# Kernel tuning notes

Measured on AMD Instinct MI355X. Metric: run time of the kernel, lower is better.

## Reference

```python
import jax, jax.numpy as jnp
import numpy as np

BLK = 64          # BLOCK_M == BLOCK_N == 64
TOPK_RATIO = 0.25


def _block_map(q, k, topk):
    # mean_pool of q blocks and mean-centered k blocks, then top-k key blocks per query block
    B, H, L, D = q.shape
    nb = L // BLK
    k_cent = k - jnp.mean(k, axis=-2, keepdims=True)
    pq = q.reshape(B, H, nb, BLK, D).mean(axis=3)          # [B,H,Mb,D]
    pk = k_cent.reshape(B, H, nb, BLK, D).mean(axis=3)     # [B,H,Nb,D]
    score = jnp.einsum('bhmd,bhnd->bhmn', pq, pk)
    _, lut = jax.lax.top_k(score, topk)                    # [B,H,Mb,topk] int32
    return lut


def reference(q, k, v):
    B, H, L, D = q.shape
    nb = L // BLK                       # M_BLOCKS == N_BLOCKS (L divisible by 64)
    topk = min(nb, int(TOPK_RATIO * nb))
    qk_scale = D ** (-0.5)

    lut = jax.lax.stop_gradient(_block_map(q, k, topk))    # routing is non-differentiable

    qb = q.reshape(B, H, nb, BLK, D)
    kb = k.reshape(B, H, nb, BLK, D)
    vb = v.reshape(B, H, nb, BLK, D)

    # gather selected key/value blocks per query block: [B,H,Mb,topk,BLK,D]
    idx = lut[:, :, :, :, None, None]
    k_sel = jnp.take_along_axis(kb[:, :, None], idx, axis=3)
    v_sel = jnp.take_along_axis(vb[:, :, None], idx, axis=3)

    # block-sparse attention restricted to the selected blocks
    s = jnp.einsum('bhmqd,bhmtkd->bhmqtk', qb, k_sel) * qk_scale
    s = s.reshape(B, H, nb, BLK, topk * BLK)
    p = jax.nn.softmax(s, axis=-1)                         # online-softmax equivalent
    v_flat = v_sel.reshape(B, H, nb, topk * BLK, D)
    o = jnp.einsum('bhmqn,bhmnd->bhmqd', p, v_flat)
    return o.reshape(B, H, L, D)


def setup_inputs() -> dict:
    key = jax.random.key(0)
    k1, k2, k3 = jax.random.split(key, 3)
    shape = (2, 8, 4096, 64)
    return {
        'q': jax.random.normal(k1, shape, dtype=jnp.float32),
        'k': jax.random.normal(k2, shape, dtype=jnp.float32),
        'v': jax.random.normal(k3, shape, dtype=jnp.float32),
    }
```

## Files before the change

### kernel.cpp

```cpp
#include <hip/hip_runtime.h>
#include <hip/hip_bf16.h>

#define B_ 2
#define H_ 8
#define L_ 4096
#define D_ 64
#define NB_ 64
#define TOPK_ 16
#define BH_ 16

typedef __bf16 bf16x8 __attribute__((ext_vector_type(8)));
typedef float f32x4 __attribute__((ext_vector_type(4)));

#if __has_builtin(__builtin_amdgcn_exp2f)
#define EXP2(x) __builtin_amdgcn_exp2f(x)
#else
#define EXP2(x) exp2f(x)
#endif

__device__ __forceinline__ void async_copy16(void* lds, const void* g) {
  __builtin_amdgcn_global_load_lds(
      (const __attribute__((address_space(1))) void*)g,
      (__attribute__((address_space(3))) void*)lds, 16, 0, 0);
}

__global__ __launch_bounds__(256) void prep_all_kernel(
    const float* __restrict__ q, const float* __restrict__ k,
    const float* __restrict__ v,
    float* __restrict__ pq, float* __restrict__ pk,
    __bf16* __restrict__ kswz, __bf16* __restrict__ vimg) {
  const int tid = threadIdx.x;
  if (blockIdx.x < BH_ * NB_) {
    const int blk = blockIdx.x;
    const int bh = blk >> 6, m = blk & 63;
    const int d = tid & 63, g = tid >> 6;
    const float* qb = q + ((size_t)bh * L_ + m * 64 + g * 16) * D_ + d;
    float sq = 0.f;
#pragma unroll
    for (int i = 0; i < 16; i++) sq += qb[(size_t)i * D_];
    __shared__ float bufq[4][64];
    bufq[g][d] = sq;
    __syncthreads();
    if (g == 0) {
      float tq = bufq[0][d] + bufq[1][d] + bufq[2][d] + bufq[3][d];
      pq[(size_t)blk * 64 + d] = tq * (1.f / 64.f);
    }
  } else if (blockIdx.x < 2 * BH_ * NB_) {
    const int blk = blockIdx.x - BH_ * NB_;
    const int srow = tid >> 2;
    const int sc16 = (tid & 3) * 16;
    __shared__ __align__(16) float s_kf[64][64];

    const float* ks = k + (size_t)blk * 4096 + srow * 64 + sc16;
    float kf[16];
#pragma unroll
    for (int h = 0; h < 4; h++) {
      float4 t4 = *(const float4*)(ks + h * 4);
      kf[h * 4 + 0] = t4.x; kf[h * 4 + 1] = t4.y; kf[h * 4 + 2] = t4.z; kf[h * 4 + 3] = t4.w;
      *(float4*)&s_kf[srow][sc16 + h * 4] = t4;
    }

    __bf16* gk = kswz + (size_t)blk * 4096;
#pragma unroll
    for (int h = 0; h < 2; h++) {
      int c8 = (sc16 >> 3) + h;
      bf16x8 kw;
#pragma unroll
      for (int j = 0; j < 8; j++) kw[j] = (__bf16)kf[h * 8 + j];
      *(bf16x8*)(gk + srow * 64 + ((c8 ^ (srow & 7)) << 3)) = kw;
    }
    __syncthreads();

    const int d = tid & 63, g = tid >> 6;
    float sk = 0.f;
#pragma unroll
    for (int i = 0; i < 16; i++) sk += s_kf[g * 16 + i][d];
    __shared__ float bufk[4][64];
    bufk[g][d] = sk;
    __syncthreads();
    if (g == 0) {
      float tk = bufk[0][d] + bufk[1][d] + bufk[2][d] + bufk[3][d];
      pk[(size_t)blk * 64 + d] = tk * (1.f / 64.f);
    }
  } else {
    const int blk = blockIdx.x - 2 * BH_ * NB_;
    const int srow = tid >> 2;
    const int sc16 = (tid & 3) * 16;

    const float* vs = v + (size_t)blk * 4096 + srow * 64 + sc16;
    float vf[16];
#pragma unroll
    for (int h = 0; h < 4; h++) {
      float4 u4 = *(const float4*)(vs + h * 4);
      vf[h * 4 + 0] = u4.x; vf[h * 4 + 1] = u4.y; vf[h * 4 + 2] = u4.z; vf[h * 4 + 3] = u4.w;
    }

    const int kpos = (srow & 32) + ((srow >> 2) & 3) * 8 + ((srow >> 4) & 1) * 4 + (srow & 3);
    __shared__ __align__(16) __bf16 s_vt[4096];
#pragma unroll
    for (int i = 0; i < 16; i++) {
      int d = sc16 + i;
      s_vt[d * 64 + kpos] = (__bf16)vf[i];
    }
    __syncthreads();
    __bf16* gv = vimg + (size_t)blk * 4096;
#pragma unroll
    for (int h = 0; h < 2; h++) {
      int c = tid + h * 256;
      int i = c >> 6, ln = c & 63;
      int ct2 = i & 3, s2 = i >> 2;
      int d = ct2 * 16 + (ln & 15), c8 = s2 * 4 + (ln >> 4);
      *(bf16x8*)(gv + c * 8) = *(const bf16x8*)(s_vt + d * 64 + c8 * 8);
    }
  }
}

__global__ __launch_bounds__(256) void blockmap_kernel(
    const float* __restrict__ pq, const float* __restrict__ pk,
    int* __restrict__ lut) {
  const int g = blockIdx.x;
  const int bh = g >> 2, q4 = g & 3;
  const int t = threadIdx.x;
  const int lane = t & 63, w = t >> 6;

  __shared__ float s_pk[64][65];
  __shared__ float s_km[64];
  __shared__ float s_pq[16][64];
  __shared__ float s_sc[4][64];

#pragma unroll
  for (int i = 0; i < 16; i++) {
    int idx = i * 256 + t;
    s_pk[idx >> 6][idx & 63] = pk[(size_t)bh * 4096 + idx];
  }
#pragma unroll
  for (int i = 0; i < 4; i++) {
    int idx = i * 256 + t;
    s_pq[idx >> 6][idx & 63] = pq[(size_t)bh * 4096 + q4 * 1024 + idx];
  }
  __syncthreads();
  if (t < 64) {
    float s = 0.f;
#pragma unroll 8
    for (int r = 0; r < 64; r++) s += s_pk[r][t];
    s_km[t] = s * (1.f / 64.f);
  }
  __syncthreads();

#pragma unroll
  for (int rr = 0; rr < 4; rr++) {
    const int row = w * 4 + rr;
    float sc = 0.f;
#pragma unroll 8
    for (int d2 = 0; d2 < 64; ++d2)
      sc += s_pq[row][d2] * (s_pk[lane][d2] - s_km[d2]);
    s_sc[w][lane] = sc;
    __syncthreads();
    int rank = 0;
#pragma unroll 8
    for (int j = 0; j < 64; j++) {
      float o = s_sc[w][j];
      rank += (o > sc) || (o == sc && j < lane);
    }
    if (rank < TOPK_)
      lut[((size_t)bh * 64 + q4 * 16 + row) * TOPK_ + rank] = lane;
    __syncthreads();
  }
}

__global__ __launch_bounds__(256) void sparse_attn_fast(
    const float* __restrict__ q, const __bf16* __restrict__ kswz,
    const __bf16* __restrict__ vimg, const float* __restrict__ pq,
    const float* __restrict__ pk, float* __restrict__ out) {
  const int bid = blockIdx.x;
  const int blk = (bid & 7) * 128 + (bid >> 3);
  const int bh = blk >> 6, m = blk & 63;
  const int tid = threadIdx.x;
  const int lane = tid & 63;
  const int w = tid >> 6;
  const int l16 = lane & 15, lhi = lane >> 4;

  __shared__ __align__(16) __bf16 Kb[2][2][4096];
  __shared__ float s_km[64];
  __shared__ float s_pqr[64];
  __shared__ float s_sc[64];
  __shared__ int s_lut[TOPK_];

  {
    float (*s_pk)[65] = (float(*)[65]) & Kb[0][0][0];
    const float* pkb = pk + (size_t)bh * 4096;
#pragma unroll
    for (int i = 0; i < 16; i++) {
      int idx = i * 256 + tid;
      s_pk[idx >> 6][idx & 63] = pkb[idx];
    }
    if (tid < 64) s_pqr[tid] = pq[((size_t)bh * 64 + m) * 64 + tid];
    __syncthreads();
    if (tid < 64) {
      float s = 0.f;
#pragma unroll 8
      for (int r = 0; r < 64; r++) s += s_pk[r][tid];
      s_km[tid] = s * (1.f / 64.f);
    }
    __syncthreads();
    float sc = 0.f;
#pragma unroll 8
    for (int d2 = 0; d2 < 64; ++d2)
      sc += s_pqr[d2] * (s_pk[lane][d2] - s_km[d2]);
    s_sc[lane] = sc;
    __syncthreads();
    int rank = 0;
#pragma unroll 8
    for (int j = 0; j < 64; j++) {
      float o = s_sc[j];
      rank += (o > sc) || (o == sc && j < lane);
    }
    if (rank < TOPK_) s_lut[rank] = lane;
    __syncthreads();
  }

  const size_t base = (size_t)bh * L_ * D_;
  const __bf16* kimg = kswz + (size_t)bh * 64 * 4096;
  const __bf16* vbase = vimg + (size_t)bh * 64 * 4096;

  const float QSC = 0.125f * 1.44269504088896340736f;
  bf16x8 qf[2];
  {
    const float* qrow = q + base + (size_t)(m * 64 + w * 16 + l16) * D_;
#pragma unroll
    for (int s = 0; s < 2; s++) {
      const float* p0 = qrow + s * 32 + lhi * 8;
      float4 a = *(const float4*)p0;
      float4 b = *(const float4*)(p0 + 4);
      bf16x8 f;
      f[0] = (__bf16)(a.x * QSC); f[1] = (__bf16)(a.y * QSC);
      f[2] = (__bf16)(a.z * QSC); f[3] = (__bf16)(a.w * QSC);
      f[4] = (__bf16)(b.x * QSC); f[5] = (__bf16)(b.y * QSC);
      f[6] = (__bf16)(b.z * QSC); f[7] = (__bf16)(b.w * QSC);
      qf[s] = f;
    }
  }

  f32x4 acc_o[4];
#pragma unroll
  for (int i = 0; i < 4; i++) acc_o[i] = (f32x4){0.f, 0.f, 0.f, 0.f};
  float l_run = 0.f;

  auto stagePair = [&](int b, int ka, int kb2) {
    const __bf16* g0 = kimg + (size_t)ka * 4096;
    const __bf16* g1 = kimg + (size_t)kb2 * 4096;
    async_copy16(&Kb[b][0][0 * 2048 + w * 512], g0 + 0 * 2048 + tid * 8);
    async_copy16(&Kb[b][0][1 * 2048 + w * 512], g0 + 1 * 2048 + tid * 8);
    async_copy16(&Kb[b][1][0 * 2048 + w * 512], g1 + 0 * 2048 + tid * 8);
    async_copy16(&Kb[b][1][1 * 2048 + w * 512], g1 + 1 * 2048 + tid * 8);
  };

  stagePair(0, s_lut[0], s_lut[1]);
  __syncthreads();

  for (int i = 0; i < 8; ++i) {
    const int cur = i & 1;
    if (i) __builtin_amdgcn_s_barrier();

    const int ka = s_lut[2 * i], kb2 = s_lut[2 * i + 1];

    const __bf16* gv0 = vbase + (size_t)ka * 4096 + lane * 8;
    bf16x8 vf0[8];
#pragma unroll
    for (int j = 0; j < 8; j++) vf0[j] = *(const bf16x8*)(gv0 + j * 512);

    asm volatile("s_waitcnt vmcnt(8)" ::: "memory");

    {
      const __bf16* Kl = &Kb[cur][0][0];
      f32x4 accs[4];
#pragma unroll
      for (int x = 0; x < 4; x++) accs[x] = (f32x4){0.f, 0.f, 0.f, 0.f};
      __builtin_amdgcn_s_setprio(1);
#pragma unroll
      for (int ct = 0; ct < 4; ct++) {
        const int key = ct * 16 + l16;
#pragma unroll
        for (int s = 0; s < 2; s++) {
          const int c8 = s * 4 + lhi;
          bf16x8 bk = *(const bf16x8*)&Kl[key * 64 + ((c8 ^ (key & 7)) << 3)];
          accs[ct] = __builtin_amdgcn_mfma_f32_16x16x32_bf16(bk, qf[s], accs[ct], 0, 0, 0);
        }
      }
      __builtin_amdgcn_s_setprio(0);
      bf16x8 pa0, pa1;
      float ls0 = 0.f, ls1 = 0.f;
#pragma unroll
      for (int j = 0; j < 8; j++) {
        float e0 = EXP2(accs[(j >> 2)][j & 3]);
        float e1 = EXP2(accs[2 + (j >> 2)][j & 3]);
        pa0[j] = (__bf16)e0; pa1[j] = (__bf16)e1;
        ls0 += e0; ls1 += e1;
      }
      l_run += ls0 + ls1;
      __builtin_amdgcn_s_setprio(1);
#pragma unroll
      for (int ct2 = 0; ct2 < 4; ct2++) {
        acc_o[ct2] = __builtin_amdgcn_mfma_f32_16x16x32_bf16(pa0, vf0[ct2], acc_o[ct2], 0, 0, 0);
        acc_o[ct2] = __builtin_amdgcn_mfma_f32_16x16x32_bf16(pa1, vf0[4 + ct2], acc_o[ct2], 0, 0, 0);
      }
      __builtin_amdgcn_s_setprio(0);
    }

    const __bf16* gv1 = vbase + (size_t)kb2 * 4096 + lane * 8;
    bf16x8 vf1[8];
#pragma unroll
    for (int j = 0; j < 8; j++) vf1[j] = *(const bf16x8*)(gv1 + j * 512);

    if (i + 1 < 8) stagePair(cur ^ 1, s_lut[2 * i + 2], s_lut[2 * i + 3]);

    {
      const __bf16* Kl = &Kb[cur][1][0];
      f32x4 accs[4];
#pragma unroll
      for (int x = 0; x < 4; x++) accs[x] = (f32x4){0.f, 0.f, 0.f, 0.f};
      __builtin_amdgcn_s_setprio(1);
#pragma unroll
      for (int ct = 0; ct < 4; ct++) {
        const int key = ct * 16 + l16;
#pragma unroll
        for (int s = 0; s < 2; s++) {
          const int c8 = s * 4 + lhi;
          bf16x8 bk = *(const bf16x8*)&Kl[key * 64 + ((c8 ^ (key & 7)) << 3)];
          accs[ct] = __builtin_amdgcn_mfma_f32_16x16x32_bf16(bk, qf[s], accs[ct], 0, 0, 0);
        }
      }
      __builtin_amdgcn_s_setprio(0);
      bf16x8 pa0, pa1;
      float ls0 = 0.f, ls1 = 0.f;
#pragma unroll
      for (int j = 0; j < 8; j++) {
        float e0 = EXP2(accs[(j >> 2)][j & 3]);
        float e1 = EXP2(accs[2 + (j >> 2)][j & 3]);
        pa0[j] = (__bf16)e0; pa1[j] = (__bf16)e1;
        ls0 += e0; ls1 += e1;
      }
      l_run += ls0 + ls1;
      __builtin_amdgcn_s_setprio(1);
#pragma unroll
      for (int ct2 = 0; ct2 < 4; ct2++) {
        acc_o[ct2] = __builtin_amdgcn_mfma_f32_16x16x32_bf16(pa0, vf1[ct2], acc_o[ct2], 0, 0, 0);
        acc_o[ct2] = __builtin_amdgcn_mfma_f32_16x16x32_bf16(pa1, vf1[4 + ct2], acc_o[ct2], 0, 0, 0);
      }
      __builtin_amdgcn_s_setprio(0);
    }
  }

  l_run += __shfl_xor(l_run, 16, 64);
  l_run += __shfl_xor(l_run, 32, 64);
  float rq[4];
#pragma unroll
  for (int r = 0; r < 4; r++)
    rq[r] = 1.f / __shfl(l_run, (lane & 48) | (lhi * 4 + r), 64);

  float* ob = out + base + (size_t)(m * 64 + w * 16) * D_;
#pragma unroll
  for (int ct2 = 0; ct2 < 4; ct2++) {
#pragma unroll
    for (int r = 0; r < 4; r++) {
      const int row = lhi * 4 + r, col = ct2 * 16 + l16;
      ob[(size_t)row * D_ + col] = acc_o[ct2][r] * rq[r];
    }
  }
}

__global__ __launch_bounds__(256) void block_means_kernel(
    const float* __restrict__ q, const float* __restrict__ k,
    float* __restrict__ pq, float* __restrict__ pk) {
  const int blk = blockIdx.x;
  const int bh = blk >> 6, m = blk & 63;
  const int d = threadIdx.x & 63, g = threadIdx.x >> 6;
  const float* qb = q + ((size_t)bh * L_ + m * 64 + g * 16) * D_ + d;
  const float* kb = k + ((size_t)bh * L_ + m * 64 + g * 16) * D_ + d;
  float sq = 0.f, sk = 0.f;
#pragma unroll
  for (int i = 0; i < 16; i++) { sq += qb[(size_t)i * D_]; sk += kb[(size_t)i * D_]; }
  __shared__ float bufq[4][64];
  __shared__ float bufk[4][64];
  bufq[g][d] = sq; bufk[g][d] = sk;
  __syncthreads();
  if (g == 0) {
    float tq = bufq[0][d] + bufq[1][d] + bufq[2][d] + bufq[3][d];
    float tk = bufk[0][d] + bufk[1][d] + bufk[2][d] + bufk[3][d];
    pq[(size_t)blk * 64 + d] = tq * (1.f / 64.f);
    pk[(size_t)blk * 64 + d] = tk * (1.f / 64.f);
  }
}

__global__ __launch_bounds__(256) void sparse_attn_slow(
    const float* __restrict__ q, const float* __restrict__ k,
    const float* __restrict__ v, const int* __restrict__ lut,
    float* __restrict__ out) {
  const int blk = blockIdx.x;
  const int bh = blk >> 6, m = blk & 63;
  const int tid = threadIdx.x;
  const int lane = tid & 63;
  const int w = tid >> 6;
  const int l16 = lane & 15, lhi = lane >> 4;

  __shared__ __align__(16) __bf16 Kl[64 * 64];
  __shared__ __align__(16) __bf16 Vt[64 * 64];
  __shared__ __align__(16) __bf16 Pl[4][16 * 64];

  const size_t base = (size_t)bh * L_ * D_;

  bf16x8 qf[2];
  {
    const float* qrow = q + base + (size_t)(m * 64 + w * 16 + l16) * D_;
#pragma unroll
    for (int s = 0; s < 2; s++) {
      const float* p0 = qrow + s * 32 + lhi * 8;
      float4 a = *(const float4*)p0;
      float4 b = *(const float4*)(p0 + 4);
      bf16x8 f;
      f[0] = (__bf16)(a.x * 0.125f); f[1] = (__bf16)(a.y * 0.125f);
      f[2] = (__bf16)(a.z * 0.125f); f[3] = (__bf16)(a.w * 0.125f);
      f[4] = (__bf16)(b.x * 0.125f); f[5] = (__bf16)(b.y * 0.125f);
      f[6] = (__bf16)(b.z * 0.125f); f[7] = (__bf16)(b.w * 0.125f);
      qf[s] = f;
    }
  }

  f32x4 acc_o[4];
#pragma unroll
  for (int i = 0; i < 4; i++) acc_o[i] = (f32x4){0.f, 0.f, 0.f, 0.f};
  float m_run[4] = {-__builtin_inff(), -__builtin_inff(), -__builtin_inff(), -__builtin_inff()};
  float l_run[4] = {0.f, 0.f, 0.f, 0.f};

  const int srow = tid >> 2;
  const int sc16 = (tid & 3) * 16;

  for (int it = 0; it < TOPK_; ++it) {
    const int kb = lut[(size_t)blk * TOPK_ + it];
    __syncthreads();
    {
      const float* ks = k + base + (size_t)(kb * 64 + srow) * D_ + sc16;
      const float* vs = v + base + (size_t)(kb * 64 + srow) * D_ + sc16;
      float kf[16], vf[16];
#pragma unroll
      for (int h = 0; h < 4; h++) {
        float4 t4 = *(const float4*)(ks + h * 4);
        kf[h * 4 + 0] = t4.x; kf[h * 4 + 1] = t4.y; kf[h * 4 + 2] = t4.z; kf[h * 4 + 3] = t4.w;
        float4 u4 = *(const float4*)(vs + h * 4);
        vf[h * 4 + 0] = u4.x; vf[h * 4 + 1] = u4.y; vf[h * 4 + 2] = u4.z; vf[h * 4 + 3] = u4.w;
      }
#pragma unroll
      for (int h = 0; h < 2; h++) {
        int c8 = (sc16 >> 3) + h;
        bf16x8 kw;
#pragma unroll
        for (int j = 0; j < 8; j++) kw[j] = (__bf16)kf[h * 8 + j];
        *(bf16x8*)&Kl[srow * 64 + ((c8 ^ (srow & 7)) << 3)] = kw;
      }
#pragma unroll
      for (int i = 0; i < 16; i++) {
        int d = sc16 + i;
        Vt[d * 64 + (srow ^ ((d & 7) << 3))] = (__bf16)vf[i];
      }
    }
    __syncthreads();

    f32x4 accs[4];
#pragma unroll
    for (int i = 0; i < 4; i++) accs[i] = (f32x4){0.f, 0.f, 0.f, 0.f};
#pragma unroll
    for (int ct = 0; ct < 4; ct++) {
      const int key = ct * 16 + l16;
#pragma unroll
      for (int s = 0; s < 2; s++) {
        const int c8 = s * 4 + lhi;
        bf16x8 bk = *(const bf16x8*)&Kl[key * 64 + ((c8 ^ (key & 7)) << 3)];
        accs[ct] = __builtin_amdgcn_mfma_f32_16x16x32_bf16(qf[s], bk, accs[ct], 0, 0, 0);
      }
    }

    float pvals[4][4];
#pragma unroll
    for (int r = 0; r < 4; r++) {
      float mx = fmaxf(fmaxf(accs[0][r], accs[1][r]), fmaxf(accs[2][r], accs[3][r]));
#pragma unroll
      for (int off = 1; off < 16; off <<= 1) mx = fmaxf(mx, __shfl_xor(mx, off, 64));
      const float mnew = fmaxf(m_run[r], mx);
      const float scale = __expf(m_run[r] - mnew);
      float rs = 0.f;
#pragma unroll
      for (int ct = 0; ct < 4; ct++) {
        float e = __expf(accs[ct][r] - mnew);
        pvals[ct][r] = e; rs += e;
      }
#pragma unroll
      for (int off = 1; off < 16; off <<= 1) rs += __shfl_xor(rs, off, 64);
      l_run[r] = l_run[r] * scale + rs;
      m_run[r] = mnew;
#pragma unroll
      for (int ct = 0; ct < 4; ct++) acc_o[ct][r] *= scale;
    }

#pragma unroll
    for (int ct = 0; ct < 4; ct++) {
#pragma unroll
      for (int r = 0; r < 4; r++) {
        const int row = lhi * 4 + r, col = ct * 16 + l16;
        Pl[w][row * 64 + (col ^ ((row & 7) << 3))] = (__bf16)pvals[ct][r];
      }
    }
#pragma unroll
    for (int s = 0; s < 2; s++) {
      const int c8 = s * 4 + lhi;
      bf16x8 pa = *(const bf16x8*)&Pl[w][l16 * 64 + ((c8 ^ (l16 & 7)) << 3)];
#pragma unroll
      for (int ct2 = 0; ct2 < 4; ct2++) {
        const int d = ct2 * 16 + l16;
        bf16x8 bv = *(const bf16x8*)&Vt[d * 64 + ((c8 ^ (d & 7)) << 3)];
        acc_o[ct2] = __builtin_amdgcn_mfma_f32_16x16x32_bf16(pa, bv, acc_o[ct2], 0, 0, 0);
      }
    }
  }

  float* ob = out + base + (size_t)(m * 64 + w * 16) * D_;
#pragma unroll
  for (int ct2 = 0; ct2 < 4; ct2++) {
#pragma unroll
    for (int r = 0; r < 4; r++) {
      const int row = lhi * 4 + r, col = ct2 * 16 + l16;
      ob[(size_t)row * D_ + col] = acc_o[ct2][r] / l_run[r];
    }
  }
}

extern "C" void kernel_launch(void* const* d_in, const int* in_sizes, int n_in,
                              void* d_out, int out_size, void* d_ws, size_t ws_size,
                              hipStream_t stream) {
  const float* q = (const float*)d_in[0];
  const float* k = (const float*)d_in[1];
  const float* v = (const float*)d_in[2];
  float* out = (float*)d_out;

  float* pq = (float*)d_ws;
  float* pk = pq + (size_t)BH_ * NB_ * D_;
  int*   lut = (int*)(pk + (size_t)BH_ * NB_ * D_);
  char*  extra = (char*)(lut + (size_t)BH_ * NB_ * TOPK_);
  __bf16* kswz = (__bf16*)extra;
  __bf16* vimg = kswz + (size_t)BH_ * NB_ * 4096;

  const size_t needed = (size_t)((char*)(vimg + (size_t)BH_ * NB_ * 4096) - (char*)d_ws);
  const bool fast = ws_size >= needed;

  if (fast) {
    hipLaunchKernelGGL(prep_all_kernel, dim3(3 * BH_ * NB_), dim3(256), 0, stream,
                       q, k, v, pq, pk, kswz, vimg);
    hipLaunchKernelGGL(sparse_attn_fast, dim3(BH_ * NB_), dim3(256), 0, stream,
                       q, kswz, vimg, pq, pk, out);
  } else {
    hipLaunchKernelGGL(block_means_kernel, dim3(BH_ * NB_), dim3(256), 0, stream, q, k, pq, pk);
    hipLaunchKernelGGL(blockmap_kernel, dim3(BH_ * 4), dim3(256), 0, stream, pq, pk, lut);
    hipLaunchKernelGGL(sparse_attn_slow, dim3(BH_ * NB_), dim3(256), 0, stream, q, k, v, lut, out);
  }
}
```

Measured before the change: 51.95 us.

## Prepack K into MFMA fragment order and load directly to registers

The prep kernel now writes K blocks in a per-lane MFMA fragment layout (staged through shared memory), so the attention kernel loads K fragments straight from global memory into registers like V, dropping the LDS double buffer, async LDS copies and barriers. The main loop becomes a simple per-block loop over the 16 selected blocks, and launch bounds request 4 blocks per CU for more occupancy. The tradeoff is losing explicit prefetch overlap: each iteration issues its K and V global loads and then waits on them, relying on occupancy to hide latency.

```diff
diff --git a/kernel.cpp b/kernel.cpp
--- a/kernel.cpp
+++ b/kernel.cpp
@@ -18,17 +18,11 @@
 #define EXP2(x) exp2f(x)
 #endif
 
-__device__ __forceinline__ void async_copy16(void* lds, const void* g) {
-  __builtin_amdgcn_global_load_lds(
-      (const __attribute__((address_space(1))) void*)g,
-      (__attribute__((address_space(3))) void*)lds, 16, 0, 0);
-}
-
 __global__ __launch_bounds__(256) void prep_all_kernel(
     const float* __restrict__ q, const float* __restrict__ k,
     const float* __restrict__ v,
     float* __restrict__ pq, float* __restrict__ pk,
-    __bf16* __restrict__ kswz, __bf16* __restrict__ vimg) {
+    __bf16* __restrict__ kimg, __bf16* __restrict__ vimg) {
   const int tid = threadIdx.x;
   if (blockIdx.x < BH_ * NB_) {
     const int blk = blockIdx.x;
@@ -50,6 +44,7 @@
     const int srow = tid >> 2;
     const int sc16 = (tid & 3) * 16;
     __shared__ __align__(16) float s_kf[64][64];
+    __shared__ __align__(16) __bf16 s_kt[4096];
 
     const float* ks = k + (size_t)blk * 4096 + srow * 64 + sc16;
     float kf[16];
@@ -60,16 +55,21 @@
       *(float4*)&s_kf[srow][sc16 + h * 4] = t4;
     }
 
-    __bf16* gk = kswz + (size_t)blk * 4096;
 #pragma unroll
     for (int h = 0; h < 2; h++) {
-      int c8 = (sc16 >> 3) + h;
+      const int d0 = sc16 + h * 8;
+      const int i = (d0 >> 5) * 4 + (srow >> 4);
+      const int ln = ((d0 >> 3) & 3) * 16 + (srow & 15);
       bf16x8 kw;
 #pragma unroll
       for (int j = 0; j < 8; j++) kw[j] = (__bf16)kf[h * 8 + j];
-      *(bf16x8*)(gk + srow * 64 + ((c8 ^ (srow & 7)) << 3)) = kw;
-    }
-    __syncthreads();
+      *(bf16x8*)&s_kt[(i * 64 + ln) * 8] = kw;
+    }
+    __syncthreads();
+
+    __bf16* gk = kimg + (size_t)blk * 4096;
+    *(bf16x8*)(gk + tid * 8)        = *(const bf16x8*)(s_kt + tid * 8);
+    *(bf16x8*)(gk + 2048 + tid * 8) = *(const bf16x8*)(s_kt + 2048 + tid * 8);
 
     const int d = tid & 63, g = tid >> 6;
     float sk = 0.f;
@@ -168,8 +168,8 @@
   }
 }
 
-__global__ __launch_bounds__(256) void sparse_attn_fast(
-    const float* __restrict__ q, const __bf16* __restrict__ kswz,
+__global__ __launch_bounds__(256, 4) void sparse_attn_fast(
+    const float* __restrict__ q, const __bf16* __restrict__ kimg,
     const __bf16* __restrict__ vimg, const float* __restrict__ pq,
     const float* __restrict__ pk, float* __restrict__ out) {
   const int bid = blockIdx.x;
@@ -180,14 +180,13 @@
   const int w = tid >> 6;
   const int l16 = lane & 15, lhi = lane >> 4;
 
-  __shared__ __align__(16) __bf16 Kb[2][2][4096];
+  __shared__ float s_pk[64][65];
   __shared__ float s_km[64];
   __shared__ float s_pqr[64];
   __shared__ float s_sc[64];
   __shared__ int s_lut[TOPK_];
 
   {
-    float (*s_pk)[65] = (float(*)[65]) & Kb[0][0][0];
     const float* pkb = pk + (size_t)bh * 4096;
 #pragma unroll
     for (int i = 0; i < 16; i++) {
@@ -220,7 +219,7 @@
   }
 
   const size_t base = (size_t)bh * L_ * D_;
-  const __bf16* kimg = kswz + (size_t)bh * 64 * 4096;
+  const __bf16* kbase = kimg + (size_t)bh * 64 * 4096;
   const __bf16* vbase = vimg + (size_t)bh * 64 * 4096;
 
   const float QSC = 0.125f * 1.44269504088896340736f;
@@ -246,109 +245,47 @@
   for (int i = 0; i < 4; i++) acc_o[i] = (f32x4){0.f, 0.f, 0.f, 0.f};
   float l_run = 0.f;
 
-  auto stagePair = [&](int b, int ka, int kb2) {
-    const __bf16* g0 = kimg + (size_t)ka * 4096;
-    const __bf16* g1 = kimg + (size_t)kb2 * 4096;
-    async_copy16(&Kb[b][0][0 * 2048 + w * 512], g0 + 0 * 2048 + tid * 8);
-    async_copy16(&Kb[b][0][1 * 2048 + w * 512], g0 + 1 * 2048 + tid * 8);
-    async_copy16(&Kb[b][1][0 * 2048 + w * 512], g1 + 0 * 2048 + tid * 8);
-    async_copy16(&Kb[b][1][1 * 2048 + w * 512], g1 + 1 * 2048 + tid * 8);
-  };
-
-  stagePair(0, s_lut[0], s_lut[1]);
-  __syncthreads();
-
-  for (int i = 0; i < 8; ++i) {
-    const int cur = i & 1;
-    if (i) __builtin_amdgcn_s_barrier();
-
-    const int ka = s_lut[2 * i], kb2 = s_lut[2 * i + 1];
-
-    const __bf16* gv0 = vbase + (size_t)ka * 4096 + lane * 8;
-    bf16x8 vf0[8];
-#pragma unroll
-    for (int j = 0; j < 8; j++) vf0[j] = *(const bf16x8*)(gv0 + j * 512);
-
-    asm volatile("s_waitcnt vmcnt(8)" ::: "memory");
-
-    {
-      const __bf16* Kl = &Kb[cur][0][0];
-      f32x4 accs[4];
-#pragma unroll
-      for (int x = 0; x < 4; x++) accs[x] = (f32x4){0.f, 0.f, 0.f, 0.f};
-      __builtin_amdgcn_s_setprio(1);
-#pragma unroll
-      for (int ct = 0; ct < 4; ct++) {
-        const int key = ct * 16 + l16;
-#pragma unroll
-        for (int s = 0; s < 2; s++) {
-          const int c8 = s * 4 + lhi;
-          bf16x8 bk = *(const bf16x8*)&Kl[key * 64 + ((c8 ^ (key & 7)) << 3)];
-          accs[ct] = __builtin_amdgcn_mfma_f32_16x16x32_bf16(bk, qf[s], accs[ct], 0, 0, 0);
-        }
-      }
-      __builtin_amdgcn_s_setprio(0);
-      bf16x8 pa0, pa1;
-      float ls0 = 0.f, ls1 = 0.f;
-#pragma unroll
-      for (int j = 0; j < 8; j++) {
-        float e0 = EXP2(accs[(j >> 2)][j & 3]);
-        float e1 = EXP2(accs[2 + (j >> 2)][j & 3]);
-        pa0[j] = (__bf16)e0; pa1[j] = (__bf16)e1;
-        ls0 += e0; ls1 += e1;
-      }
-      l_run += ls0 + ls1;
-      __builtin_amdgcn_s_setprio(1);
-#pragma unroll
-      for (int ct2 = 0; ct2 < 4; ct2++) {
-        acc_o[ct2] = __builtin_amdgcn_mfma_f32_16x16x32_bf16(pa0, vf0[ct2], acc_o[ct2], 0, 0, 0);
-        acc_o[ct2] = __builtin_amdgcn_mfma_f32_16x16x32_bf16(pa1, vf0[4 + ct2], acc_o[ct2], 0, 0, 0);
-      }
-      __builtin_amdgcn_s_setprio(0);
-    }
-
-    const __bf16* gv1 = vbase + (size_t)kb2 * 4096 + lane * 8;
-    bf16x8 vf1[8];
-#pragma unroll
-    for (int j = 0; j < 8; j++) vf1[j] = *(const bf16x8*)(gv1 + j * 512);
-
-    if (i + 1 < 8) stagePair(cur ^ 1, s_lut[2 * i + 2], s_lut[2 * i + 3]);
-
-    {
-      const __bf16* Kl = &Kb[cur][1][0];
-      f32x4 accs[4];
-#pragma unroll
-      for (int x = 0; x < 4; x++) accs[x] = (f32x4){0.f, 0.f, 0.f, 0.f};
-      __builtin_amdgcn_s_setprio(1);
-#pragma unroll
-      for (int ct = 0; ct < 4; ct++) {
-        const int key = ct * 16 + l16;
-#pragma unroll
-        for (int s = 0; s < 2; s++) {
-          const int c8 = s * 4 + lhi;
-          bf16x8 bk = *(const bf16x8*)&Kl[key * 64 + ((c8 ^ (key & 7)) << 3)];
-          accs[ct] = __builtin_amdgcn_mfma_f32_16x16x32_bf16(bk, qf[s], accs[ct], 0, 0, 0);
-        }
-      }
-      __builtin_amdgcn_s_setprio(0);
-      bf16x8 pa0, pa1;
-      float ls0 = 0.f, ls1 = 0.f;
-#pragma unroll
-      for (int j = 0; j < 8; j++) {
-        float e0 = EXP2(accs[(j >> 2)][j & 3]);
-        float e1 = EXP2(accs[2 + (j >> 2)][j & 3]);
-        pa0[j] = (__bf16)e0; pa1[j] = (__bf16)e1;
-        ls0 += e0; ls1 += e1;
-      }
-      l_run += ls0 + ls1;
-      __builtin_amdgcn_s_setprio(1);
-#pragma unroll
-      for (int ct2 = 0; ct2 < 4; ct2++) {
-        acc_o[ct2] = __builtin_amdgcn_mfma_f32_16x16x32_bf16(pa0, vf1[ct2], acc_o[ct2], 0, 0, 0);
-        acc_o[ct2] = __builtin_amdgcn_mfma_f32_16x16x32_bf16(pa1, vf1[4 + ct2], acc_o[ct2], 0, 0, 0);
-      }
-      __builtin_amdgcn_s_setprio(0);
-    }
+  for (int it = 0; it < TOPK_; ++it) {
+    const int kb = s_lut[it];
+
+    const __bf16* gk = kbase + (size_t)kb * 4096 + lane * 8;
+    const __bf16* gv = vbase + (size_t)kb * 4096 + lane * 8;
+    bf16x8 kf[8], vf[8];
+#pragma unroll
+    for (int j = 0; j < 8; j++) kf[j] = *(const bf16x8*)(gk + j * 512);
+#pragma unroll
+    for (int j = 0; j < 8; j++) vf[j] = *(const bf16x8*)(gv + j * 512);
+
+    f32x4 accs[4];
+#pragma unroll
+    for (int x = 0; x < 4; x++) accs[x] = (f32x4){0.f, 0.f, 0.f, 0.f};
+    __builtin_amdgcn_s_setprio(1);
+#pragma unroll
+    for (int ct = 0; ct < 4; ct++) {
+#pragma unroll
+      for (int s = 0; s < 2; s++)
+        accs[ct] = __builtin_amdgcn_mfma_f32_16x16x32_bf16(kf[s * 4 + ct], qf[s], accs[ct], 0, 0, 0);
+    }
+    __builtin_amdgcn_s_setprio(0);
+
+    bf16x8 pa0, pa1;
+    float ls0 = 0.f, ls1 = 0.f;
+#pragma unroll
+    for (int j = 0; j < 8; j++) {
+      float e0 = EXP2(accs[(j >> 2)][j & 3]);
+      float e1 = EXP2(accs[2 + (j >> 2)][j & 3]);
+      pa0[j] = (__bf16)e0; pa1[j] = (__bf16)e1;
+      ls0 += e0; ls1 += e1;
+    }
+    l_run += ls0 + ls1;
+
+    __builtin_amdgcn_s_setprio(1);
+#pragma unroll
+    for (int ct2 = 0; ct2 < 4; ct2++) {
+      acc_o[ct2] = __builtin_amdgcn_mfma_f32_16x16x32_bf16(pa0, vf[ct2], acc_o[ct2], 0, 0, 0);
+      acc_o[ct2] = __builtin_amdgcn_mfma_f32_16x16x32_bf16(pa1, vf[4 + ct2], acc_o[ct2], 0, 0, 0);
+    }
+    __builtin_amdgcn_s_setprio(0);
   }
 
   l_run += __shfl_xor(l_run, 16, 64);
@@ -545,17 +482,17 @@
   float* pk = pq + (size_t)BH_ * NB_ * D_;
   int*   lut = (int*)(pk + (size_t)BH_ * NB_ * D_);
   char*  extra = (char*)(lut + (size_t)BH_ * NB_ * TOPK_);
-  __bf16* kswz = (__bf16*)extra;
-  __bf16* vimg = kswz + (size_t)BH_ * NB_ * 4096;
+  __bf16* kimg = (__bf16*)extra;
+  __bf16* vimg = kimg + (size_t)BH_ * NB_ * 4096;
 
   const size_t needed = (size_t)((char*)(vimg + (size_t)BH_ * NB_ * 4096) - (char*)d_ws);
   const bool fast = ws_size >= needed;
 
   if (fast) {
     hipLaunchKernelGGL(prep_all_kernel, dim3(3 * BH_ * NB_), dim3(256), 0, stream,
-                       q, k, v, pq, pk, kswz, vimg);
+                       q, k, v, pq, pk, kimg, vimg);
     hipLaunchKernelGGL(sparse_attn_fast, dim3(BH_ * NB_), dim3(256), 0, stream,
-                       q, kswz, vimg, pq, pk, out);
+                       q, kimg, vimg, pq, pk, out);
   } else {
     hipLaunchKernelGGL(block_means_kernel, dim3(BH_ * NB_), dim3(256), 0, stream, q, k, pq, pk);
     hipLaunchKernelGGL(blockmap_kernel, dim3(BH_ * 4), dim3(256), 0, stream, pq, pk, lut);
```

New measurement: 54.45 us. +4.8%, slower.
